# Optimization experiments

Measured on AMD Instinct MI355X. Metric: run time of the kernel, lower is better.

The kernel has to match this reference:

```python
import jax, jax.numpy as jnp
import numpy as np

B, T, D = 2, 1024, 1024
E, H, TOPK = 32, 256, 4
S, HS = 2, H * TOPK  # shared experts, shared hidden dim


def setup_inputs() -> dict:
    key = jax.random.key(0)
    ks = jax.random.split(key, 10)
    sc = 0.02
    return {
        "x": jax.random.normal(ks[0], (B, T, D), dtype=jnp.float32),
        "Wr": jax.random.normal(ks[1], (E, D), dtype=jnp.float32) * sc,
        "router_bias": jnp.zeros((E,), dtype=jnp.float32),
        "Wg": jax.random.normal(ks[2], (E, H, D), dtype=jnp.float32) * sc,
        "Wu": jax.random.normal(ks[3], (E, H, D), dtype=jnp.float32) * sc,
        "Wd": jax.random.normal(ks[4], (E, D, H), dtype=jnp.float32) * sc,
        "Sg": jax.random.normal(ks[5], (S, HS, D), dtype=jnp.float32) * sc,
        "Su": jax.random.normal(ks[6], (S, HS, D), dtype=jnp.float32) * sc,
        "Sd": jax.random.normal(ks[7], (S, D, HS), dtype=jnp.float32) * sc,
    }


def reference(x, Wr, router_bias, Wg, Wu, Wd, Sg, Su, Sd):
    Bx, Tx, Dx = x.shape
    flat = x.reshape(-1, Dx)                      # [N, D]
    N = flat.shape[0]

    # Router: softmax over raw logits, top-k selection on biased logits
    logits = flat @ Wr.T                          # [N, E]
    scores = jax.nn.softmax(logits, axis=-1)
    _, topk_idx = jax.lax.top_k(logits + router_bias, TOPK)   # [N, K]
    topk_scores = jnp.take_along_axis(scores, topk_idx, axis=-1)
    topk_scores = topk_scores / jnp.sum(topk_scores, axis=-1, keepdims=True)

    # Dense per-token per-expert combine weights (0 for unselected experts)
    cw = jnp.zeros((N, E), dtype=flat.dtype).at[
        jnp.arange(N)[:, None], topk_idx
    ].add(topk_scores)                            # [N, E]

    # Routed experts: SwiGLU applied per expert, zero-weighted if unselected
    g = jnp.einsum("nd,ehd->neh", flat, Wg)       # [N, E, H]
    u = jnp.einsum("nd,ehd->neh", flat, Wu)
    h = jax.nn.silu(g) * u
    hw = h * cw[:, :, None]                       # fold combine weight before down-proj
    out = jnp.einsum("neh,edh->nd", hw, Wd)       # [N, D]

    # Shared experts: always active, summed on top
    gs = jnp.einsum("nd,shd->nsh", flat, Sg)      # [N, S, HS]
    us = jnp.einsum("nd,shd->nsh", flat, Su)
    hs = jax.nn.silu(gs) * us
    out = out + jnp.einsum("nsh,sdh->nd", hs, Sd)

    return out.reshape(Bx, Tx, Dx)
```

## Files before the change

### kernel.cpp

```cpp
#include <hip/hip_runtime.h>
#include <hip/hip_bf16.h>


#define N_TOK 2048
#define DDIM 1024
#define NEXP 32
#define HDIM 256
#define TOPK 4
#define NSH 2
#define HSH 1024
#define CNTS 32
#define WMAX 160
#define WM2  96

typedef unsigned short us4 __attribute__((ext_vector_type(4)));
typedef unsigned short us8 __attribute__((ext_vector_type(8)));
typedef short bf16x8 __attribute__((ext_vector_type(8)));
typedef float f32x4 __attribute__((ext_vector_type(4)));

__device__ __forceinline__ unsigned short f2bf(float f) {
  union { float f; unsigned u; } v; v.f = f;
  unsigned r = v.u + 0x7fffu + ((v.u >> 16) & 1u);
  return (unsigned short)(r >> 16);
}
__device__ __forceinline__ float bf2f(unsigned short h) {
  union { unsigned u; float f; } v; v.u = ((unsigned)h) << 16; return v.f;
}
__device__ __forceinline__ uint2 cvt4u(float4 v) {
  union { __hip_bfloat162 b; unsigned u; } a, b2;
  a.b  = __float22bfloat162_rn(make_float2(v.x, v.y));
  b2.b = __float22bfloat162_rn(make_float2(v.z, v.w));
  return make_uint2(a.u, b2.u);
}

__device__ __forceinline__ void pipe_barrier() {
  asm volatile("s_waitcnt lgkmcnt(0)" ::: "memory");
  __builtin_amdgcn_s_barrier();
  __builtin_amdgcn_sched_barrier(0);
}

#define C_X4   524288L
#define C_WG4  2621440L
#define C_WU4  4718592L
#define C_WD4  6815744L
#define C_SG4  7340032L
#define C_SU4  7864320L
#define C_TOT4 8388608L
#define NCVT   16384

__global__ __launch_bounds__(256) void k_prep(const float* __restrict__ x,
                                              const float* __restrict__ Wr,
                                              const float* __restrict__ rb,
                                              const float* __restrict__ Wg,
                                              const float* __restrict__ Wu,
                                              const float* __restrict__ Wd,
                                              const float* __restrict__ Sg,
                                              const float* __restrict__ Su,
                                              const float* __restrict__ Sd,
                                              unsigned short* __restrict__ xb,
                                              unsigned short* __restrict__ Wgb,
                                              unsigned short* __restrict__ Wub,
                                              unsigned short* __restrict__ Wdb,
                                              unsigned short* __restrict__ Sgb,
                                              unsigned short* __restrict__ Sub,
                                              unsigned short* __restrict__ Sdb,
                                              int* __restrict__ cnt,
                                              int* __restrict__ ent,
                                              float* __restrict__ wgt) {
  __shared__ float sX[8 * 1024];
  __shared__ float sLog[8 * 32];
  int tid = threadIdx.x;
  if (blockIdx.x >= 256) {
    long base = (long)(blockIdx.x - 256) * 512;
    const float* s; unsigned short* d; long off;
    if (base < C_WG4) {
      if (base < C_X4)  { s = x;  d = xb;  off = base; }
      else              { s = Wg; d = Wgb; off = base - C_X4; }
    } else if (base < C_WD4) {
      if (base < C_WU4) { s = Wu; d = Wub; off = base - C_WG4; }
      else              { s = Wd; d = Wdb; off = base - C_WU4; }
    } else if (base < C_SU4) {
      if (base < C_SG4) { s = Sg; d = Sgb; off = base - C_WD4; }
      else              { s = Su; d = Sub; off = base - C_SG4; }
    } else              { s = Sd; d = Sdb; off = base - C_SU4; }
    long i0 = off + tid;
    long i1 = i0 + 256;
    float4 v0 = reinterpret_cast<const float4*>(s)[i0];
    float4 v1 = reinterpret_cast<const float4*>(s)[i1];
    reinterpret_cast<uint2*>(d)[i0] = cvt4u(v0);
    reinterpret_cast<uint2*>(d)[i1] = cvt4u(v1);
    return;
  }
  int blk = blockIdx.x;
  {
    const float4* xsrc = reinterpret_cast<const float4*>(x + (size_t)blk * 8 * 1024);
    float4* xdst = reinterpret_cast<float4*>(sX);
#pragma unroll
    for (int i = 0; i < 8; i++) xdst[tid + 256 * i] = xsrc[tid + 256 * i];
  }
  __syncthreads();
  int tloc = tid >> 5, e = tid & 31;
  const float4* wr4 = reinterpret_cast<const float4*>(Wr + (size_t)e * DDIM);
  const float* xr = sX + tloc * 1024;
  float acc = 0.f;
#pragma unroll 8
  for (int d4 = 0; d4 < 256; d4++) {
    float4 wv = wr4[d4];
    acc += xr[d4 * 4 + 0] * wv.x + xr[d4 * 4 + 1] * wv.y +
           xr[d4 * 4 + 2] * wv.z + xr[d4 * 4 + 3] * wv.w;
  }
  sLog[tloc * 32 + e] = acc;
  __syncthreads();
  if (tid < 8) {
    int tok = blk * 8 + tid;
    const float* lg = sLog + tid * 32;
    int usedmask = 0;
    int idx[TOPK]; float lv[TOPK];
#pragma unroll
    for (int k = 0; k < TOPK; k++) {
      float best = -3.4e38f; int bi = 0;
      for (int ee = 0; ee < NEXP; ee++) {
        if ((usedmask >> ee) & 1) continue;
        float v = lg[ee] + rb[ee];
        if (v > best) { best = v; bi = ee; }
      }
      usedmask |= 1 << bi; idx[k] = bi; lv[k] = lg[bi];
    }
    float m = fmaxf(fmaxf(lv[0], lv[1]), fmaxf(lv[2], lv[3]));
    float w[TOPK]; float ssum = 0.f;
#pragma unroll
    for (int k = 0; k < TOPK; k++) { w[k] = __expf(lv[k] - m); ssum += w[k]; }
    float inv = 1.f / ssum;
#pragma unroll
    for (int k = 0; k < TOPK; k++) {
      int ee = idx[k];
      int pos = atomicAdd(&cnt[ee * CNTS], 1);
      ent[ee * N_TOK + pos] = tok * TOPK + k;
      wgt[ee * N_TOK + pos] = w[k] * inv;
    }
  }
}

__global__ void k_plan(const int* __restrict__ cnt, int* __restrict__ wk, int* __restrict__ nwk,
                       int* __restrict__ wk2, int* __restrict__ nwk2) {
  if (threadIdx.x != 0) return;
  int w = 0, w2 = 0;
  for (int e = 0; e < NEXP; e++) {
    int ne = cnt[e * CNTS];
    int nt = (ne + 63) >> 6;
    for (int t = 0; t < nt; t++) wk[w++] = e | (t << 8);
    int nt2 = (ne + 127) >> 7;
    for (int t = 0; t < nt2; t++) wk2[w2++] = e | (t << 8);
  }
  nwk[0] = w;
  nwk2[0] = w2;
}

__global__ __launch_bounds__(512) void k_routed_gu(const unsigned short* __restrict__ xb,
                                                   const unsigned short* __restrict__ Wgb,
                                                   const unsigned short* __restrict__ Wub,
                                                   const int* __restrict__ cnt,
                                                   const int* __restrict__ ent,
                                                   const float* __restrict__ wgt,
                                                   unsigned short* __restrict__ hw,
                                                   const int* __restrict__ wk2,
                                                   const int* __restrict__ nwk2) {
  int widx = blockIdx.x;
  if (widx >= nwk2[0]) return;
  int item = wk2[widx];
  int e = item & 255, mt = item >> 8, ht = blockIdx.y;
  int ne = cnt[e * CNTS];
  __shared__ unsigned short sA[2][128 * 40];
  __shared__ unsigned short sB[2][128 * 40];
  __shared__ int sTok[128];
  __shared__ float sW[128];
  int tid = threadIdx.x, lane = tid & 63, wid = tid >> 6;
  int wm = wid >> 2, wn = wid & 3;
  if (tid < 128) {
    int pos = mt * 128 + tid;
    int p2 = min(pos, ne - 1);
    sTok[tid] = ent[e * N_TOK + p2];
    sW[tid] = (pos < ne) ? wgt[e * N_TOK + p2] : 0.f;
  }
  __syncthreads();

  int ar = tid >> 2, akc = tid & 3;
  const unsigned short* aSrc = xb + (size_t)(sTok[ar] >> 2) * DDIM + akc * 8;
  int aOff = ar * 40 + akc * 8;
  int br = tid >> 2, bkc = tid & 3;
  int sel = (br >> 4) & 1;
  int h = ht * 64 + ((br >> 5) << 4) + (br & 15);
  const unsigned short* bSrc = (sel ? Wub : Wgb) + (size_t)(e * HDIM + h) * DDIM + bkc * 8;
  int bOff = br * 40 + bkc * 8;

  us8 aReg = *reinterpret_cast<const us8*>(aSrc);
  us8 bReg = *reinterpret_cast<const us8*>(bSrc);

  f32x4 acc[4][2];
#pragma unroll
  for (int mf = 0; mf < 4; mf++)
#pragma unroll
    for (int nf = 0; nf < 2; nf++) acc[mf][nf] = {0.f, 0.f, 0.f, 0.f};

  int cur = 0;
  for (int step = 0; step < 32; ++step) {
    *reinterpret_cast<us8*>(&sA[cur][aOff]) = aReg;
    *reinterpret_cast<us8*>(&sB[cur][bOff]) = bReg;
    if (step < 31) {
      int k0 = (step + 1) * 32;
      aReg = *reinterpret_cast<const us8*>(aSrc + k0);
      bReg = *reinterpret_cast<const us8*>(bSrc + k0);
    }
    pipe_barrier();
    int ka = (lane >> 4) * 8;
    bf16x8 a[4];
#pragma unroll
    for (int mf = 0; mf < 4; mf++)
      a[mf] = *reinterpret_cast<const bf16x8*>(&sA[cur][(wm * 64 + mf * 16 + (lane & 15)) * 40 + ka]);
#pragma unroll
    for (int nf = 0; nf < 2; nf++) {
      bf16x8 b = *reinterpret_cast<const bf16x8*>(&sB[cur][(wn * 32 + nf * 16 + (lane & 15)) * 40 + ka]);
#pragma unroll
      for (int mf = 0; mf < 4; mf++)
        acc[mf][nf] = __builtin_amdgcn_mfma_f32_16x16x32_bf16(a[mf], b, acc[mf][nf], 0, 0, 0);
    }
    cur ^= 1;
  }
#pragma unroll
  for (int mf = 0; mf < 4; mf++) {
#pragma unroll
    for (int r = 0; r < 4; r++) {
      int tl = wm * 64 + mf * 16 + ((lane >> 4) << 2) + r;
      int pos = mt * 128 + tl;
      if (pos < ne) {
        float g = acc[mf][0][r], u = acc[mf][1][r];
        float hval = (g / (1.f + __expf(-g))) * u * sW[tl];
        int ts = sTok[tl];
        int hcol = ht * 64 + wn * 16 + (lane & 15);
        hw[(size_t)ts * HDIM + hcol] = f2bf(hval);
      }
    }
  }
}

__global__ __launch_bounds__(256) void k_routed_down(const unsigned short* __restrict__ hw,
                                                     const unsigned short* __restrict__ Wdb,
                                                     const int* __restrict__ cnt,
                                                     const int* __restrict__ ent,
                                                     unsigned short* __restrict__ Pslot,
                                                     const int* __restrict__ wk,
                                                     const int* __restrict__ nwk) {
  int widx = blockIdx.x;
  if (widx >= nwk[0]) return;
  int item = wk[widx];
  int e = item & 255, mt = item >> 8, dh = blockIdx.y;
  int ne = cnt[e * CNTS];
  __shared__ unsigned short sA[2][64 * 40];
  __shared__ unsigned short sB[2][256 * 40];
  __shared__ int sTok[64];
  int tid = threadIdx.x, lane = tid & 63, w = tid >> 6;
  if (tid < 64) {
    int pos = mt * 64 + tid;
    int p2 = min(pos, ne - 1);
    sTok[tid] = ent[e * N_TOK + p2];
  }
  __syncthreads();

  int arow = tid >> 2, akc = tid & 3;
  const unsigned short* aSrc = hw + (size_t)sTok[arow] * HDIM + akc * 8;
  int aOff = arow * 40 + akc * 8;
  const unsigned short* bSrc[4];
  int bOff[4];
#pragma unroll
  for (int p = 0; p < 4; p++) {
    int c = tid + p * 256;
    int row = c >> 2, kc = c & 3;
    int d = dh * 256 + row;
    bSrc[p] = Wdb + (size_t)(e * DDIM + d) * HDIM + kc * 8;
    bOff[p] = row * 40 + kc * 8;
  }

  us8 aReg = *reinterpret_cast<const us8*>(aSrc);
  us8 bReg[4];
#pragma unroll
  for (int p = 0; p < 4; p++) bReg[p] = *reinterpret_cast<const us8*>(bSrc[p]);

  f32x4 acc[16];
#pragma unroll
  for (int f = 0; f < 16; f++) acc[f] = {0.f, 0.f, 0.f, 0.f};

  int cur = 0;
  for (int step = 0; step < 8; ++step) {
    *reinterpret_cast<us8*>(&sA[cur][aOff]) = aReg;
#pragma unroll
    for (int p = 0; p < 4; p++) *reinterpret_cast<us8*>(&sB[cur][bOff[p]]) = bReg[p];
    if (step < 7) {
      int k0 = (step + 1) * 32;
      aReg = *reinterpret_cast<const us8*>(aSrc + k0);
#pragma unroll
      for (int p = 0; p < 4; p++) bReg[p] = *reinterpret_cast<const us8*>(bSrc[p] + k0);
    }
    pipe_barrier();
    int ka = (lane >> 4) * 8;
    bf16x8 a = *reinterpret_cast<const bf16x8*>(&sA[cur][(w * 16 + (lane & 15)) * 40 + ka]);
#pragma unroll
    for (int f = 0; f < 16; f++) {
      bf16x8 b = *reinterpret_cast<const bf16x8*>(&sB[cur][(f * 16 + (lane & 15)) * 40 + ka]);
      acc[f] = __builtin_amdgcn_mfma_f32_16x16x32_bf16(a, b, acc[f], 0, 0, 0);
    }
    cur ^= 1;
  }
#pragma unroll
  for (int f = 0; f < 16; f++) {
#pragma unroll
    for (int r = 0; r < 4; r++) {
      int tl = w * 16 + ((lane >> 4) << 2) + r;
      int pos = mt * 64 + tl;
      if (pos < ne) {
        int ts = sTok[tl];
        int d = dh * 256 + f * 16 + (lane & 15);
        Pslot[(size_t)ts * DDIM + d] = f2bf(acc[f][r]);
      }
    }
  }
}

__global__ __launch_bounds__(512) void k_shared_gu(const unsigned short* __restrict__ xb,
                                                   const unsigned short* __restrict__ Sgb,
                                                   const unsigned short* __restrict__ Sub,
                                                   unsigned short* __restrict__ hs) {
  int s = blockIdx.x >> 3, ht = blockIdx.x & 7;
  int mt = blockIdx.y;
  __shared__ unsigned short sA[2][128 * 40];
  __shared__ unsigned short sB[2][256 * 40];
  int tid = threadIdx.x, lane = tid & 63, wid = tid >> 6;
  int wm = wid >> 2, wn = wid & 3;

  int ar = tid >> 2, akc = tid & 3;
  const unsigned short* aSrc = xb + (size_t)(mt * 128 + ar) * DDIM + akc * 8;
  int aOff = ar * 40 + akc * 8;
  const unsigned short* bSrc[2];
  int bOff[2];
#pragma unroll
  for (int p = 0; p < 2; p++) {
    int c = tid + p * 512;
    int row = c >> 2, kc = c & 3;
    int sel = (row >> 4) & 1;
    int h = ht * 128 + ((row >> 5) << 4) + (row & 15);
    bSrc[p] = (sel ? Sub : Sgb) + (size_t)(s * HSH + h) * DDIM + kc * 8;
    bOff[p] = row * 40 + kc * 8;
  }

  us8 aReg = *reinterpret_cast<const us8*>(aSrc);
  us8 bReg[2];
#pragma unroll
  for (int p = 0; p < 2; p++) bReg[p] = *reinterpret_cast<const us8*>(bSrc[p]);

  f32x4 acc[4][4];
#pragma unroll
  for (int mf = 0; mf < 4; mf++)
#pragma unroll
    for (int nf = 0; nf < 4; nf++) acc[mf][nf] = {0.f, 0.f, 0.f, 0.f};

  int cur = 0;
  for (int step = 0; step < 32; ++step) {
    *reinterpret_cast<us8*>(&sA[cur][aOff]) = aReg;
#pragma unroll
    for (int p = 0; p < 2; p++) *reinterpret_cast<us8*>(&sB[cur][bOff[p]]) = bReg[p];
    if (step < 31) {
      int k0 = (step + 1) * 32;
      aReg = *reinterpret_cast<const us8*>(aSrc + k0);
#pragma unroll
      for (int p = 0; p < 2; p++) bReg[p] = *reinterpret_cast<const us8*>(bSrc[p] + k0);
    }
    pipe_barrier();
    int ka = (lane >> 4) * 8;
    bf16x8 a[4];
#pragma unroll
    for (int mf = 0; mf < 4; mf++)
      a[mf] = *reinterpret_cast<const bf16x8*>(&sA[cur][(wm * 64 + mf * 16 + (lane & 15)) * 40 + ka]);
#pragma unroll
    for (int nf = 0; nf < 4; nf++) {
      bf16x8 b = *reinterpret_cast<const bf16x8*>(&sB[cur][(wn * 64 + nf * 16 + (lane & 15)) * 40 + ka]);
#pragma unroll
      for (int mf = 0; mf < 4; mf++)
        acc[mf][nf] = __builtin_amdgcn_mfma_f32_16x16x32_bf16(a[mf], b, acc[mf][nf], 0, 0, 0);
    }
    cur ^= 1;
  }
#pragma unroll
  for (int mf = 0; mf < 4; mf++) {
#pragma unroll
    for (int t = 0; t < 2; t++) {
#pragma unroll
      for (int r = 0; r < 4; r++) {
        int tok = mt * 128 + wm * 64 + mf * 16 + ((lane >> 4) << 2) + r;
        float g = acc[mf][2 * t][r], u = acc[mf][2 * t + 1][r];
        float hval = (g / (1.f + __expf(-g))) * u;
        int h = ht * 128 + (wn * 2 + t) * 16 + (lane & 15);
        hs[(size_t)(tok * NSH + s) * HSH + h] = f2bf(hval);
      }
    }
  }
}

__global__ __launch_bounds__(512) void k_shared_down(const unsigned short* __restrict__ hs,
                                                     const unsigned short* __restrict__ Sdb,
                                                     unsigned short* __restrict__ Psh) {
  int dh = blockIdx.x >> 1, s = blockIdx.x & 1;
  int mt = blockIdx.y;
  __shared__ unsigned short sA[2][128 * 40];
  __shared__ unsigned short sB[2][128 * 40];
  int tid = threadIdx.x, lane = tid & 63, wid = tid >> 6;
  int wm = wid >> 2, wn = wid & 3;

  int ar = tid >> 2, akc = tid & 3;
  const unsigned short* aSrc = hs + (size_t)((mt * 128 + ar) * NSH + s) * HSH + akc * 8;
  int aOff = ar * 40 + akc * 8;
  int br = tid >> 2, bkc = tid & 3;
  const unsigned short* bSrc = Sdb + (size_t)(s * DDIM + dh * 128 + br) * HSH + bkc * 8;
  int bOff = br * 40 + bkc * 8;

  us8 aReg = *reinterpret_cast<const us8*>(aSrc);
  us8 bReg = *reinterpret_cast<const us8*>(bSrc);

  f32x4 acc[4][2];
#pragma unroll
  for (int mf = 0; mf < 4; mf++)
#pragma unroll
    for (int nf = 0; nf < 2; nf++) acc[mf][nf] = {0.f, 0.f, 0.f, 0.f};

  int cur = 0;
  for (int step = 0; step < 32; ++step) {
    *reinterpret_cast<us8*>(&sA[cur][aOff]) = aReg;
    *reinterpret_cast<us8*>(&sB[cur][bOff]) = bReg;
    if (step < 31) {
      int k0 = (step + 1) * 32;
      aReg = *reinterpret_cast<const us8*>(aSrc + k0);
      bReg = *reinterpret_cast<const us8*>(bSrc + k0);
    }
    pipe_barrier();
    int ka = (lane >> 4) * 8;
    bf16x8 a[4];
#pragma unroll
    for (int mf = 0; mf < 4; mf++)
      a[mf] = *reinterpret_cast<const bf16x8*>(&sA[cur][(wm * 64 + mf * 16 + (lane & 15)) * 40 + ka]);
#pragma unroll
    for (int nf = 0; nf < 2; nf++) {
      bf16x8 b = *reinterpret_cast<const bf16x8*>(&sB[cur][(wn * 32 + nf * 16 + (lane & 15)) * 40 + ka]);
#pragma unroll
      for (int mf = 0; mf < 4; mf++)
        acc[mf][nf] = __builtin_amdgcn_mfma_f32_16x16x32_bf16(a[mf], b, acc[mf][nf], 0, 0, 0);
    }
    cur ^= 1;
  }
#pragma unroll
  for (int mf = 0; mf < 4; mf++) {
#pragma unroll
    for (int nf = 0; nf < 2; nf++) {
#pragma unroll
      for (int r = 0; r < 4; r++) {
        int tok = mt * 128 + wm * 64 + mf * 16 + ((lane >> 4) << 2) + r;
        int d = dh * 128 + wn * 32 + nf * 16 + (lane & 15);
        Psh[(size_t)s * N_TOK * DDIM + (size_t)tok * DDIM + d] = f2bf(acc[mf][nf][r]);
      }
    }
  }
}

__global__ __launch_bounds__(256) void k_combine(const unsigned short* __restrict__ Pslot,
                                                 const unsigned short* __restrict__ Psh,
                                                 float* __restrict__ out) {
  int i = blockIdx.x * 256 + threadIdx.x;
  int base = i * 8;
  int tok = base >> 10, d = base & 1023;
  const us8 p0 = *reinterpret_cast<const us8*>(Pslot + ((size_t)tok * 4 + 0) * DDIM + d);
  const us8 p1 = *reinterpret_cast<const us8*>(Pslot + ((size_t)tok * 4 + 1) * DDIM + d);
  const us8 p2 = *reinterpret_cast<const us8*>(Pslot + ((size_t)tok * 4 + 2) * DDIM + d);
  const us8 p3 = *reinterpret_cast<const us8*>(Pslot + ((size_t)tok * 4 + 3) * DDIM + d);
  const us8 q0 = *reinterpret_cast<const us8*>(Psh + (size_t)base);
  const us8 q1 = *reinterpret_cast<const us8*>(Psh + (size_t)N_TOK * DDIM + base);
  float o[8];
#pragma unroll
  for (int j = 0; j < 8; j++)
    o[j] = bf2f(p0[j]) + bf2f(p1[j]) + bf2f(p2[j]) + bf2f(p3[j]) + bf2f(q0[j]) + bf2f(q1[j]);
  float4 v0 = {o[0], o[1], o[2], o[3]};
  float4 v1 = {o[4], o[5], o[6], o[7]};
  reinterpret_cast<float4*>(out + base)[0] = v0;
  reinterpret_cast<float4*>(out + base)[1] = v1;
}

extern "C" void kernel_launch(void* const* d_in, const int* in_sizes, int n_in,
                              void* d_out, int out_size, void* d_ws, size_t ws_size,
                              hipStream_t stream) {
  const float* x  = (const float*)d_in[0];
  const float* Wr = (const float*)d_in[1];
  const float* rb = (const float*)d_in[2];
  const float* Wg = (const float*)d_in[3];
  const float* Wu = (const float*)d_in[4];
  const float* Wd = (const float*)d_in[5];
  const float* Sg = (const float*)d_in[6];
  const float* Su = (const float*)d_in[7];
  const float* Sd = (const float*)d_in[8];
  float* out = (float*)d_out;
  char* w = (char*)d_ws;

  unsigned short* xb    = (unsigned short*)(w + (size_t)0);
  unsigned short* Wgb   = (unsigned short*)(w + ((size_t)4  << 20));
  unsigned short* Wub   = (unsigned short*)(w + ((size_t)20 << 20));
  unsigned short* Wdb   = (unsigned short*)(w + ((size_t)36 << 20));
  unsigned short* Sgb   = (unsigned short*)(w + ((size_t)52 << 20));
  unsigned short* Sub   = (unsigned short*)(w + ((size_t)56 << 20));
  unsigned short* Sdb   = (unsigned short*)(w + ((size_t)60 << 20));
  unsigned short* hw    = (unsigned short*)(w + ((size_t)64 << 20));
  unsigned short* hs    = (unsigned short*)(w + ((size_t)68 << 20));
  unsigned short* Pslot = (unsigned short*)(w + ((size_t)76 << 20));
  unsigned short* Psh   = (unsigned short*)(w + ((size_t)92 << 20));
  int*   cnt = (int*)(w + ((size_t)100 << 20));
  int*   ent = (int*)(w + ((size_t)100 << 20) + 8192);
  float* wgt = (float*)(w + ((size_t)100 << 20) + 8192 + (size_t)NEXP * N_TOK * 4);
  int*   wk   = (int*)(w + ((size_t)102 << 20));
  int*   nwk  = (int*)(w + ((size_t)102 << 20) + 4096);
  int*   wk2  = (int*)(w + ((size_t)102 << 20) + 8192);
  int*   nwk2 = (int*)(w + ((size_t)102 << 20) + 12288);

  hipMemsetAsync(cnt, 0, NEXP * CNTS * sizeof(int), stream);

  k_prep<<<256 + NCVT, 256, 0, stream>>>(x, Wr, rb, Wg, Wu, Wd, Sg, Su, Sd,
                                         xb, Wgb, Wub, Wdb, Sgb, Sub, Sdb,
                                         cnt, ent, wgt);
  k_plan<<<1, 64, 0, stream>>>(cnt, wk, nwk, wk2, nwk2);

  k_routed_gu<<<dim3(WM2, 4), 512, 0, stream>>>(xb, Wgb, Wub, cnt, ent, wgt, hw, wk2, nwk2);
  k_routed_down<<<dim3(WMAX, 4), 256, 0, stream>>>(hw, Wdb, cnt, ent, Pslot, wk, nwk);

  k_shared_gu<<<dim3(16, 16), 512, 0, stream>>>(xb, Sgb, Sub, hs);
  k_shared_down<<<dim3(16, 16), 512, 0, stream>>>(hs, Sdb, Psh);

  k_combine<<<N_TOK * DDIM / (256 * 8), 256, 0, stream>>>(Pslot, Psh, out);
}
```

Baseline: 164.2 us.

## Retile routed down-proj to 128x128 tiles with 8 waves; vectorize bf16 conversion stores

The routed down-projection now uses 128-token by 128-column tiles with 512 threads arranged as a 2x4 wave grid, driven by the 128-row work list, instead of 64x256 tiles with 4 waves. This gives each wave a 4x2 MFMA fragment block, which improves A/B register reuse and raises the number of waves per block. It also reduces per-thread B loads and accumulator registers, in exchange for more blocks along D. Separately, the fp32-to-bf16 conversion now has each thread handle two adjacent float4s and emit one 16-byte store instead of two 8-byte stores.

Result: no change. 161.9 us (-1.4%).

```diff
diff --git a/kernel.cpp b/kernel.cpp
--- a/kernel.cpp
+++ b/kernel.cpp
@@ -83,12 +83,12 @@
       if (base < C_SG4) { s = Sg; d = Sgb; off = base - C_WD4; }
       else              { s = Su; d = Sub; off = base - C_SG4; }
     } else              { s = Sd; d = Sdb; off = base - C_SU4; }
-    long i0 = off + tid;
-    long i1 = i0 + 256;
+    long i0 = off + 2 * tid;
     float4 v0 = reinterpret_cast<const float4*>(s)[i0];
-    float4 v1 = reinterpret_cast<const float4*>(s)[i1];
-    reinterpret_cast<uint2*>(d)[i0] = cvt4u(v0);
-    reinterpret_cast<uint2*>(d)[i1] = cvt4u(v1);
+    float4 v1 = reinterpret_cast<const float4*>(s)[i0 + 1];
+    uint2 a = cvt4u(v0), b = cvt4u(v1);
+    uint4 o = make_uint4(a.x, a.y, b.x, b.y);
+    reinterpret_cast<uint4*>(d)[(off >> 1) + tid] = o;
     return;
   }
   int blk = blockIdx.x;
@@ -243,83 +243,84 @@
   }
 }
 
-__global__ __launch_bounds__(256) void k_routed_down(const unsigned short* __restrict__ hw,
+__global__ __launch_bounds__(512) void k_routed_down(const unsigned short* __restrict__ hw,
                                                      const unsigned short* __restrict__ Wdb,
                                                      const int* __restrict__ cnt,
                                                      const int* __restrict__ ent,
                                                      unsigned short* __restrict__ Pslot,
-                                                     const int* __restrict__ wk,
-                                                     const int* __restrict__ nwk) {
+                                                     const int* __restrict__ wk2,
+                                                     const int* __restrict__ nwk2) {
   int widx = blockIdx.x;
-  if (widx >= nwk[0]) return;
-  int item = wk[widx];
+  if (widx >= nwk2[0]) return;
+  int item = wk2[widx];
   int e = item & 255, mt = item >> 8, dh = blockIdx.y;
   int ne = cnt[e * CNTS];
-  __shared__ unsigned short sA[2][64 * 40];
-  __shared__ unsigned short sB[2][256 * 40];
-  __shared__ int sTok[64];
-  int tid = threadIdx.x, lane = tid & 63, w = tid >> 6;
-  if (tid < 64) {
-    int pos = mt * 64 + tid;
+  __shared__ unsigned short sA[2][128 * 40];
+  __shared__ unsigned short sB[2][128 * 40];
+  __shared__ int sTok[128];
+  int tid = threadIdx.x, lane = tid & 63, wid = tid >> 6;
+  int wm = wid >> 2, wn = wid & 3;
+  if (tid < 128) {
+    int pos = mt * 128 + tid;
     int p2 = min(pos, ne - 1);
     sTok[tid] = ent[e * N_TOK + p2];
   }
   __syncthreads();
 
-  int arow = tid >> 2, akc = tid & 3;
-  const unsigned short* aSrc = hw + (size_t)sTok[arow] * HDIM + akc * 8;
-  int aOff = arow * 40 + akc * 8;
-  const unsigned short* bSrc[4];
-  int bOff[4];
-#pragma unroll
-  for (int p = 0; p < 4; p++) {
-    int c = tid + p * 256;
-    int row = c >> 2, kc = c & 3;
-    int d = dh * 256 + row;
-    bSrc[p] = Wdb + (size_t)(e * DDIM + d) * HDIM + kc * 8;
-    bOff[p] = row * 40 + kc * 8;
-  }
+  int ar = tid >> 2, akc = tid & 3;
+  const unsigned short* aSrc = hw + (size_t)sTok[ar] * HDIM + akc * 8;
+  int aOff = ar * 40 + akc * 8;
+  int br = tid >> 2, bkc = tid & 3;
+  int d0 = dh * 128 + br;
+  const unsigned short* bSrc = Wdb + (size_t)(e * DDIM + d0) * HDIM + bkc * 8;
+  int bOff = br * 40 + bkc * 8;
 
   us8 aReg = *reinterpret_cast<const us8*>(aSrc);
-  us8 bReg[4];
-#pragma unroll
-  for (int p = 0; p < 4; p++) bReg[p] = *reinterpret_cast<const us8*>(bSrc[p]);
-
-  f32x4 acc[16];
-#pragma unroll
-  for (int f = 0; f < 16; f++) acc[f] = {0.f, 0.f, 0.f, 0.f};
+  us8 bReg = *reinterpret_cast<const us8*>(bSrc);
+
+  f32x4 acc[4][2];
+#pragma unroll
+  for (int mf = 0; mf < 4; mf++)
+#pragma unroll
+    for (int nf = 0; nf < 2; nf++) acc[mf][nf] = {0.f, 0.f, 0.f, 0.f};
 
   int cur = 0;
   for (int step = 0; step < 8; ++step) {
     *reinterpret_cast<us8*>(&sA[cur][aOff]) = aReg;
-#pragma unroll
-    for (int p = 0; p < 4; p++) *reinterpret_cast<us8*>(&sB[cur][bOff[p]]) = bReg[p];
+    *reinterpret_cast<us8*>(&sB[cur][bOff]) = bReg;
     if (step < 7) {
       int k0 = (step + 1) * 32;
       aReg = *reinterpret_cast<const us8*>(aSrc + k0);
-#pragma unroll
-      for (int p = 0; p < 4; p++) bReg[p] = *reinterpret_cast<const us8*>(bSrc[p] + k0);
+      bReg = *reinterpret_cast<const us8*>(bSrc + k0);
     }
     pipe_barrier();
     int ka = (lane >> 4) * 8;
-    bf16x8 a = *reinterpret_cast<const bf16x8*>(&sA[cur][(w * 16 + (lane & 15)) * 40 + ka]);
-#pragma unroll
-    for (int f = 0; f < 16; f++) {
-      bf16x8 b = *reinterpret_cast<const bf16x8*>(&sB[cur][(f * 16 + (lane & 15)) * 40 + ka]);
-      acc[f] = __builtin_amdgcn_mfma_f32_16x16x32_bf16(a, b, acc[f], 0, 0, 0);
+    bf16x8 a[4];
+#pragma unroll
+    for (int mf = 0; mf < 4; mf++)
+      a[mf] = *reinterpret_cast<const bf16x8*>(&sA[cur][(wm * 64 + mf * 16 + (lane & 15)) * 40 + ka]);
+#pragma unroll
+    for (int nf = 0; nf < 2; nf++) {
+      bf16x8 b = *reinterpret_cast<const bf16x8*>(&sB[cur][(wn * 32 + nf * 16 + (lane & 15)) * 40 + ka]);
+#pragma unroll
+      for (int mf = 0; mf < 4; mf++)
+        acc[mf][nf] = __builtin_amdgcn_mfma_f32_16x16x32_bf16(a[mf], b, acc[mf][nf], 0, 0, 0);
     }
     cur ^= 1;
   }
 #pragma unroll
-  for (int f = 0; f < 16; f++) {
-#pragma unroll
-    for (int r = 0; r < 4; r++) {
-      int tl = w * 16 + ((lane >> 4) << 2) + r;
-      int pos = mt * 64 + tl;
-      if (pos < ne) {
-        int ts = sTok[tl];
-        int d = dh * 256 + f * 16 + (lane & 15);
-        Pslot[(size_t)ts * DDIM + d] = f2bf(acc[f][r]);
+  for (int mf = 0; mf < 4; mf++) {
+#pragma unroll
+    for (int nf = 0; nf < 2; nf++) {
+#pragma unroll
+      for (int r = 0; r < 4; r++) {
+        int tl = wm * 64 + mf * 16 + ((lane >> 4) << 2) + r;
+        int pos = mt * 128 + tl;
+        if (pos < ne) {
+          int ts = sTok[tl];
+          int d = dh * 128 + wn * 32 + nf * 16 + (lane & 15);
+          Pslot[(size_t)ts * DDIM + d] = f2bf(acc[mf][nf][r]);
+        }
       }
     }
   }
@@ -532,7 +533,7 @@
   k_plan<<<1, 64, 0, stream>>>(cnt, wk, nwk, wk2, nwk2);
 
   k_routed_gu<<<dim3(WM2, 4), 512, 0, stream>>>(xb, Wgb, Wub, cnt, ent, wgt, hw, wk2, nwk2);
-  k_routed_down<<<dim3(WMAX, 4), 256, 0, stream>>>(hw, Wdb, cnt, ent, Pslot, wk, nwk);
+  k_routed_down<<<dim3(WM2, 8), 512, 0, stream>>>(hw, Wdb, cnt, ent, Pslot, wk2, nwk2);
 
   k_shared_gu<<<dim3(16, 16), 512, 0, stream>>>(xb, Sgb, Sub, hs);
   k_shared_down<<<dim3(16, 16), 512, 0, stream>>>(hs, Sdb, Psh);
```
